# Optimization experiments

Measured on AMD Instinct MI355X. Metric: run time of the kernel, lower is better.

## Reference

```python
import jax, jax.numpy as jnp
import numpy as np

B, S, I, H, L, O = 32, 512, 1024, 1024, 3, 1024


def setup_inputs() -> dict:
    key = jax.random.key(0)
    ks = jax.random.split(key, 13)
    sc = 1.0 / np.sqrt(H)
    w = lambda k, shape: (jax.random.normal(k, shape, dtype=jnp.float32) * sc)
    return {
        "x": jax.random.normal(ks[0], (B, S, I), dtype=jnp.float32),
        "h0": jax.random.normal(ks[1], (B, L, H), dtype=jnp.float32),
        "Wzi": w(ks[2], (L, H, I)),
        "Wzh": w(ks[3], (L, H, H)),
        "bzh": w(ks[4], (L, H)),
        "Wri": w(ks[5], (L, H, I)),
        "Wrh": w(ks[6], (L, H, H)),
        "brh": w(ks[7], (L, H)),
        "Wgi": w(ks[8], (L, H, I)),
        "Wgh": w(ks[9], (L, H, H)),
        "bgh": w(ks[10], (L, H)),
        "Wout": w(ks[11], (O, H)),
        "bout": w(ks[12], (O,)),
    }


def reference(x, h0, Wzi, Wzh, bzh, Wri, Wrh, brh, Wgi, Wgh, bgh, Wout, bout):
    n_layers = Wzi.shape[0]
    # carry: hidden per layer, shape (L, B, H)
    h_init = jnp.transpose(h0, (1, 0, 2))
    x_t_major = jnp.transpose(x, (1, 0, 2))  # (S, B, I)

    def step(h, x_t):
        inp = x_t
        new_h = []
        for l in range(n_layers):
            hl = h[l]
            z = jax.nn.sigmoid(inp @ Wzi[l].T + hl @ Wzh[l].T + bzh[l])
            r = jax.nn.sigmoid(inp @ Wri[l].T + hl @ Wrh[l].T + brh[l])
            g = jnp.tanh(inp @ Wgi[l].T + r * (hl @ Wgh[l].T + bgh[l]))
            hn = z * hl + (1.0 - z) * g  # update gate keeps old state
            new_h.append(hn)
            inp = hn
        out_t = inp @ Wout.T + bout
        return jnp.stack(new_h), out_t

    h_final, outs = jax.lax.scan(step, h_init, x_t_major)
    layer_output = jnp.transpose(outs, (1, 0, 2))   # (B, S, O)
    hidden_state = jnp.transpose(h_final, (1, 0, 2))  # (B, L, H)
    return layer_output, hidden_state
```

## Files before the change

kernel.cpp:

```cpp
#include <hip/hip_runtime.h>
#include <hip/hip_bf16.h>


#define NB 32
#define NS 512
#define NI 1024
#define NH 1024
#define NL 3
#define NO 1024

#define WGN 256
#define BLK 512
#define SLOTS 12
#define RPB 2096
#define ZROW 72
#define COFF (73 * RPB)
#define CPITCH 33
#define LDSB (COFF + 48 * CPITCH * 4)

#define GENB   (WGN * 32)
#define CLAIMB (GENB + 16 * 32)
#define DONEB  (CLAIMB + 16 * 32)
#define GFL_N  9472

using short8 = __attribute__((ext_vector_type(8))) short;
using floatx4 = __attribute__((ext_vector_type(4))) float;

static __device__ __forceinline__ float bf2f(unsigned short u) {
    union { unsigned int i; float f; } v;
    v.i = ((unsigned int)u) << 16;
    return v.f;
}

static __device__ __forceinline__ unsigned short f2bf(float f) {
    __hip_bfloat16 h = __float2bfloat16(f);
    union { __hip_bfloat16 h; unsigned short u; } v;
    v.h = h;
    return v.u;
}

static __device__ __forceinline__ void load8h(const unsigned short* p, float w[8]) {
    uint4 q = *(const uint4*)p;
    unsigned int u[4] = {q.x, q.y, q.z, q.w};
#pragma unroll
    for (int i = 0; i < 4; ++i) {
        w[2*i]   = __uint_as_float(u[i] << 16);
        w[2*i+1] = __uint_as_float(u[i] & 0xffff0000u);
    }
}

static __device__ __forceinline__ void load8f(const float* p, float w[8]) {
    float4 a = *(const float4*)p;
    float4 b = *(const float4*)(p + 4);
    w[0]=a.x; w[1]=a.y; w[2]=a.z; w[3]=a.w;
    w[4]=b.x; w[5]=b.y; w[6]=b.z; w[7]=b.w;
}

static __device__ __forceinline__ int xcc_id() {
    unsigned v;
    asm volatile("s_getreg_b32 %0, hwreg(20, 0, 32)" : "=s"(v));
    return (int)(v & 7);
}

__global__ void detect_kernel(const unsigned int* __restrict__ xw, int* __restrict__ flag) {
    __shared__ int cnt[256];
    int c = 0;
    for (int i = threadIdx.x; i < 1024; i += 256) {
        unsigned int e = (xw[i] >> 7) & 0xFFu;
        if (e >= 0x78u && e <= 0x84u) c++;
    }
    cnt[threadIdx.x] = c;
    __syncthreads();
    if (threadIdx.x == 0) {
        int s = 0;
        for (int i = 0; i < 256; ++i) s += cnt[i];
        *flag = (s < 512) ? 1 : 0;
    }
}

__global__ void init_act(const void* __restrict__ h0,
                         unsigned int* __restrict__ act,
                         unsigned int* __restrict__ gflags,
                         const int* __restrict__ flagp) {
    const int f32m = *flagp;
    const int idx = blockIdx.x * 256 + threadIdx.x;
    if (idx < GFL_N) gflags[idx] = 0u;
    if (idx >= NL * NB * NH) return;
    const int l = idx >> 15;
    const int b = (idx >> 10) & 31;
    const int j = idx & 1023;
    const size_t src = (size_t)b * NL * NH + (size_t)l * NH + j;
    float v = f32m ? ((const float*)h0)[src] : bf2f(((const unsigned short*)h0)[src]);
    unsigned short hi = f2bf(v);
    unsigned short lo = f2bf(v - bf2f(hi));
    const size_t dst = ((size_t)(l * 2 + 1) * NB + b) * NH + j;
    act[dst] = ((unsigned int)hi << 16) | lo;
}

template<int F32M>
__global__ __launch_bounds__(BLK, 2) void gru_persist(
    const void* __restrict__ x,
    const void* __restrict__ Wzi_, const void* __restrict__ Wzh_, const void* __restrict__ bzh_,
    const void* __restrict__ Wri_, const void* __restrict__ Wrh_, const void* __restrict__ brh_,
    const void* __restrict__ Wgi_, const void* __restrict__ Wgh_, const void* __restrict__ bgh_,
    void* __restrict__ dout,
    unsigned int* __restrict__ act,
    float* __restrict__ stfin,
    const int* __restrict__ flagp,
    unsigned int* __restrict__ gflags)
{
    if (*flagp != F32M) return;

    extern __shared__ char lds[];
    float* clds = (float*)(lds + COFF);

    const int tid  = threadIdx.x;
    const int wg   = blockIdx.x;
    const int lane = tid & 63;
    const int wid  = tid >> 6;
    const int Mtile = wid & 1;
    const int khalf = wid >> 1;
    const int n16  = lane & 15;
    const int q4   = lane >> 4;

    const int slot0 = wg * SLOTS;

    {
        const void* Wmats[6] = {Wzi_, Wzh_, Wri_, Wrh_, Wgi_, Wgh_};
        if (F32M) {
            for (int idx = tid; idx < 72 * 256; idx += BLK) {
                const int r = idx >> 8, c4 = (idx & 255) * 4;
                const int slot = slot0 + r / 6, g = r % 6;
                const int layer = slot >> 10, j = slot & 1023;
                const float* src = (const float*)Wmats[g] + (size_t)layer * NH * NI + (size_t)j * NI + c4;
                float4 f = *(const float4*)src;
                unsigned short* dst = (unsigned short*)(lds + r * RPB + c4 * 2);
                dst[0] = f2bf(f.x); dst[1] = f2bf(f.y); dst[2] = f2bf(f.z); dst[3] = f2bf(f.w);
            }
        } else {
            for (int idx = tid; idx < 72 * 128; idx += BLK) {
                const int r = idx >> 7, c8 = (idx & 127) * 8;
                const int slot = slot0 + r / 6, g = r % 6;
                const int layer = slot >> 10, j = slot & 1023;
                const unsigned short* src = (const unsigned short*)Wmats[g] + (size_t)layer * NH * NI + (size_t)j * NI + c8;
                *(uint4*)(lds + r * RPB + c8 * 2) = *(const uint4*)src;
            }
        }
        unsigned int* z = (unsigned int*)(lds + ZROW * RPB);
        for (int c = tid; c < RPB / 4; c += BLK) z[c] = 0u;
        for (int i = tid; i < 48 * CPITCH; i += BLK) clds[i] = 0.f;
    }

    int eci = 0, eb = 0, elg = 0, ej = 0;
    float ebz = 0.f, ebr = 0.f, ebg = 0.f, ehp = 0.f;
    if (tid < NB * SLOTS) {
        eci = tid % SLOTS; eb = tid / SLOTS;
        const int slot = slot0 + eci;
        elg = slot >> 10; ej = slot & 1023;
        const size_t bidx = (size_t)elg * NH + ej;
        if (F32M) {
            ebz = ((const float*)bzh_)[bidx];
            ebr = ((const float*)brh_)[bidx];
            ebg = ((const float*)bgh_)[bidx];
        } else {
            ebz = bf2f(((const unsigned short*)bzh_)[bidx]);
            ebr = bf2f(((const unsigned short*)brh_)[bidx]);
            ebg = bf2f(((const unsigned short*)bgh_)[bidx]);
        }
    }

    const int lay0 = slot0 >> 10;
    const int lay1 = (slot0 + SLOTS - 1) >> 10;
    const int ngroups = (lay0 == lay1) ? 1 : 2;
    const int n0 = (ngroups == 1) ? SLOTS : (1024 - (slot0 & 1023));

    const int myxcd = xcc_id();
    const bool isl0 = (lay0 == 0);
    const int mb = Mtile * 16 + n16;

    short8 XH[8], XL[8];
    auto xprefetch = [&](int t) {
        if (F32M) {
            const float* xb = (const float*)x + ((size_t)mb * NS + t) * NI + khalf * 256 + q4 * 8;
#pragma unroll
            for (int ks = 0; ks < 8; ++ks) {
                float f[8];
                load8f(xb + ks * 32, f);
#pragma unroll
                for (int e = 0; e < 8; ++e) {
                    unsigned short h = f2bf(f[e]);
                    XH[ks][e] = (short)h;
                    XL[ks][e] = (short)f2bf(f[e] - bf2f(h));
                }
            }
        } else {
            const unsigned short* xb = (const unsigned short*)x + ((size_t)mb * NS + t) * NI + khalf * 256 + q4 * 8;
#pragma unroll
            for (int ks = 0; ks < 8; ++ks)
                XH[ks] = *(const short8*)(xb + ks * 32);
        }
    };
    if (isl0) xprefetch(0);

    __syncthreads();

    for (int s = 0; s < NS + NL - 1; ++s) {
        floatx4 acc[3];
#pragma unroll
        for (int nt = 0; nt < 3; ++nt) acc[nt] = (floatx4){0.f, 0.f, 0.f, 0.f};

        for (int grp = 0; grp < ngroups; ++grp) {
            const int lg = (grp == 0) ? lay0 : lay1;
            const int t = s - lg;
            if (t < 0 || t >= NS) continue;
            const int ntLo = (grp == 0) ? 0 : ((4 * n0) >> 4);
            const int ntHi = (grp == 0) ? (ngroups == 1 ? 2 : ((4 * n0) >> 4) - 1) : 2;

            for (int phase = 0; phase < 2; ++phase) {
                int brow[3];
#pragma unroll
                for (int nt = 0; nt < 3; ++nt) {
                    const int v = nt * 16 + n16;
                    const int ci = v >> 2, g = v & 3;
                    int r;
                    if (phase == 0) r = (g == 3) ? ZROW : ci * 6 + ((g == 2) ? 4 : g * 2);
                    else            r = (g == 2) ? ZROW : ci * 6 + ((g == 3) ? 5 : g * 2 + 1);
                    brow[nt] = r;
                }

                const bool isx = (phase == 0 && lg == 0);
                const bool dolo = isx ? (F32M != 0) : true;

                short8 AH[8], AL[8];
                if (isx) {
#pragma unroll
                    for (int ks = 0; ks < 8; ++ks) { AH[ks] = XH[ks]; if (F32M) AL[ks] = XL[ks]; }
                } else {
                    const int src_l = (phase == 0) ? lg - 1 : lg;
                    const int src_p = (phase == 0) ? (t & 1) : ((t - 1) & 1);
                    const size_t ab = ((size_t)(src_l * 2 + src_p) * NB + mb) * NH + khalf * 256 + q4 * 8;
                    const uint4* ap = (const uint4*)(act + ab);
                    uint4 qq[16];
#pragma unroll
                    for (int ks = 0; ks < 8; ++ks) {
                        qq[2*ks]   = ap[ks * 8];
                        qq[2*ks+1] = ap[ks * 8 + 1];
                    }
#pragma unroll
                    for (int ks = 0; ks < 8; ++ks) {
                        unsigned int c[8] = {qq[2*ks].x, qq[2*ks].y, qq[2*ks].z, qq[2*ks].w,
                                             qq[2*ks+1].x, qq[2*ks+1].y, qq[2*ks+1].z, qq[2*ks+1].w};
#pragma unroll
                        for (int e = 0; e < 8; ++e) {
                            AH[ks][e] = (short)(c[e] >> 16);
                            AL[ks][e] = (short)(c[e] & 0xffffu);
                        }
                    }
                }

#pragma unroll
                for (int ks = 0; ks < 8; ++ks) {
                    const int k0 = khalf * 256 + ks * 32;
#pragma unroll
                    for (int nt = 0; nt < 3; ++nt) {
                        if (nt < ntLo || nt > ntHi) continue;
                        const short8 bf = *(const short8*)(lds + brow[nt] * RPB + k0 * 2 + q4 * 16);
                        acc[nt] = __builtin_amdgcn_mfma_f32_16x16x32_bf16(AH[ks], bf, acc[nt], 0, 0, 0);
                        if (dolo)
                            acc[nt] = __builtin_amdgcn_mfma_f32_16x16x32_bf16(AL[ks], bf, acc[nt], 0, 0, 0);
                    }
                }
            }
        }

        {
            const int mbase = Mtile * 16 + q4 * 4;
#pragma unroll
            for (int nt = 0; nt < 3; ++nt) {
                const int vcol = nt * 16 + n16;
#pragma unroll
                for (int r = 0; r < 4; ++r)
                    atomicAdd(&clds[vcol * CPITCH + mbase + r], acc[nt][r]);
            }
        }
        __syncthreads();

        if (tid < NB * SLOTS) {
            const int t = s - elg;
            if (t >= 0 && t < NS) {
                const float zp = clds[(eci * 4 + 0) * CPITCH + eb];
                const float rp = clds[(eci * 4 + 1) * CPITCH + eb];
                const float gi = clds[(eci * 4 + 2) * CPITCH + eb];
                const float gh = clds[(eci * 4 + 3) * CPITCH + eb];
                clds[(eci * 4 + 0) * CPITCH + eb] = 0.f;
                clds[(eci * 4 + 1) * CPITCH + eb] = 0.f;
                clds[(eci * 4 + 2) * CPITCH + eb] = 0.f;
                clds[(eci * 4 + 3) * CPITCH + eb] = 0.f;
                float hp;
                if (t == 0) {
                    const size_t hoff = ((size_t)(elg * 2 + 1) * NB + eb) * NH + ej;
                    const unsigned int pv = act[hoff];
                    hp = bf2f((unsigned short)(pv >> 16)) + bf2f((unsigned short)(pv & 0xffffu));
                } else {
                    hp = ehp;
                }
                const float z = 1.f / (1.f + expf(-(zp + ebz)));
                const float r = 1.f / (1.f + expf(-(rp + ebr)));
                const float g = tanhf(gi + r * (gh + ebg));
                const float hn = z * hp + (1.f - z) * g;
                ehp = hn;
                const unsigned short hi = f2bf(hn);
                const unsigned short lo = f2bf(hn - bf2f(hi));
                const size_t woff = ((size_t)(elg * 2 + (t & 1)) * NB + eb) * NH + ej;
                __hip_atomic_store(&act[woff], ((unsigned int)hi << 16) | lo,
                                   __ATOMIC_RELAXED, __HIP_MEMORY_SCOPE_AGENT);
                if (elg == 2) {
                    const size_t o = ((size_t)eb * NS + t) * NO + ej;
                    if (F32M) ((float*)dout)[o] = hn;
                    else      ((unsigned short*)dout)[o] = f2bf(hn);
                }
                if (t == NS - 1)
                    stfin[((size_t)elg * NB + eb) * NH + ej] = hn;
            }
        }

        __syncthreads();
        if (tid == 0)
            __hip_atomic_store(&gflags[wg * 32], (unsigned int)(s + 1),
                               __ATOMIC_RELAXED, __HIP_MEMORY_SCOPE_AGENT);

        if (isl0 && (s + 1) < NS) xprefetch(s + 1);

        if (wg == 0) {
            if (tid < WGN) {
                while (__hip_atomic_load(&gflags[tid * 32], __ATOMIC_RELAXED,
                                         __HIP_MEMORY_SCOPE_AGENT) <= (unsigned int)s)
                    __builtin_amdgcn_s_sleep(1);
            }
            __syncthreads();
            if (tid < 16)
                __hip_atomic_store(&gflags[GENB + tid * 32], (unsigned int)(s + 1),
                                   __ATOMIC_RELAXED, __HIP_MEMORY_SCOPE_AGENT);
        } else {
            if (tid == 0) {
                while (__hip_atomic_load(&gflags[GENB + (wg >> 4) * 32], __ATOMIC_RELAXED,
                                         __HIP_MEMORY_SCOPE_AGENT) <= (unsigned int)s)
                    __builtin_amdgcn_s_sleep(1);
            }
        }
        if (tid == 0) {
            const unsigned tag = (unsigned)(s + 1);
            unsigned* claim = &gflags[CLAIMB + (myxcd * 2 + (s & 1)) * 32];
            unsigned old = __hip_atomic_exchange(claim, tag,
                                                 __ATOMIC_RELAXED, __HIP_MEMORY_SCOPE_AGENT);
            if (old != tag) {
                __builtin_amdgcn_fence(__ATOMIC_ACQUIRE, "agent");
                __hip_atomic_store(&gflags[DONEB + myxcd * 32], tag,
                                   __ATOMIC_RELAXED, __HIP_MEMORY_SCOPE_AGENT);
            } else {
                while (__hip_atomic_load(&gflags[DONEB + myxcd * 32], __ATOMIC_RELAXED,
                                         __HIP_MEMORY_SCOPE_AGENT) <= (unsigned int)s)
                    __builtin_amdgcn_s_sleep(1);
                asm volatile("buffer_inv" ::: "memory");
            }
            __builtin_amdgcn_sched_barrier(0);
        }
        __syncthreads();
    }
}

__global__ void init_kernel(const void* __restrict__ h0, float* __restrict__ st,
                            const int* __restrict__ flagp) {
    const int f32m = *flagp;
    const int idx = blockIdx.x * 256 + threadIdx.x;
    if (idx >= NL * NB * NH) return;
    const int l = idx >> 15;
    const int b = (idx >> 10) & 31;
    const int j = idx & 1023;
    const size_t src = (size_t)b * NL * NH + (size_t)l * NH + j;
    st[idx] = f32m ? ((const float*)h0)[src] : bf2f(((const unsigned short*)h0)[src]);
}

__global__ __launch_bounds__(256) void gru_layer(
    const void*  __restrict__ x,
    const float* __restrict__ inp,
    const float* __restrict__ hprev,
    float*       __restrict__ hnew,
    void*        __restrict__ h2out,
    const void* __restrict__ Wzi_, const void* __restrict__ Wzh_, const void* __restrict__ bzh_,
    const void* __restrict__ Wri_, const void* __restrict__ Wrh_, const void* __restrict__ brh_,
    const void* __restrict__ Wgi_, const void* __restrict__ Wgh_, const void* __restrict__ bgh_,
    const int* __restrict__ flagp, int tl, int isX)
{
    __shared__ float s_in[NB][129];
    __shared__ float s_h [NB][129];
    __shared__ float s_red[256][6];

    const int f32m = *flagp;
    const int t = tl & 0xFFFF;
    const int l = tl >> 16;
    const int tid = threadIdx.x;
    const int b   = tid & 31;
    const int jl  = (tid >> 5) & 1;
    const int ks  = tid >> 6;
    const int j   = blockIdx.x * 2 + jl;

    const size_t wIl = (size_t)l * NH * NI + (size_t)j * NI;
    const size_t bl  = (size_t)l * NH + j;

    float azi = 0.f, azh = 0.f, ari = 0.f, arh = 0.f, agi = 0.f, agh = 0.f;

    for (int kc = 0; kc < 8; ++kc) {
        const int k0 = kc * 128;
        __syncthreads();
        for (int idx = tid; idx < NB * 128; idx += 256) {
            const int r = idx >> 7, c = idx & 127;
            float vi;
            if (isX) {
                const size_t xo = (size_t)r * NS * NI + (size_t)t * NI + (k0 + c);
                vi = f32m ? ((const float*)x)[xo] : bf2f(((const unsigned short*)x)[xo]);
            } else {
                vi = inp[r * NH + k0 + c];
            }
            s_in[r][c] = vi;
            s_h [r][c] = hprev[r * NH + k0 + c];
        }
        __syncthreads();

        const int cbase = ks * 32;
#pragma unroll
        for (int q8 = 0; q8 < 4; ++q8) {
            const int c = cbase + q8 * 8;
            const int k = k0 + c;
            float wz[8], wr[8], wg[8], vz[8], vr[8], vg[8];
            if (f32m) {
                load8f((const float*)Wzi_ + wIl + k, wz);
                load8f((const float*)Wri_ + wIl + k, wr);
                load8f((const float*)Wgi_ + wIl + k, wg);
                load8f((const float*)Wzh_ + wIl + k, vz);
                load8f((const float*)Wrh_ + wIl + k, vr);
                load8f((const float*)Wgh_ + wIl + k, vg);
            } else {
                load8h((const unsigned short*)Wzi_ + wIl + k, wz);
                load8h((const unsigned short*)Wri_ + wIl + k, wr);
                load8h((const unsigned short*)Wgi_ + wIl + k, wg);
                load8h((const unsigned short*)Wzh_ + wIl + k, vz);
                load8h((const unsigned short*)Wrh_ + wIl + k, vr);
                load8h((const unsigned short*)Wgh_ + wIl + k, vg);
            }
            float ai[8], ah[8];
#pragma unroll
            for (int q = 0; q < 8; ++q) { ai[q] = s_in[b][c + q]; ah[q] = s_h[b][c + q]; }
#pragma unroll
            for (int q = 0; q < 8; ++q) {
                azi = fmaf(wz[q], ai[q], azi);
                ari = fmaf(wr[q], ai[q], ari);
                agi = fmaf(wg[q], ai[q], agi);
                azh = fmaf(vz[q], ah[q], azh);
                arh = fmaf(vr[q], ah[q], arh);
                agh = fmaf(vg[q], ah[q], agh);
            }
        }
    }

    s_red[tid][0] = azi; s_red[tid][1] = azh; s_red[tid][2] = ari;
    s_red[tid][3] = arh; s_red[tid][4] = agi; s_red[tid][5] = agh;
    __syncthreads();

    if (ks == 0) {
#pragma unroll
        for (int w = 1; w < 4; ++w) {
            azi += s_red[tid + 64*w][0]; azh += s_red[tid + 64*w][1];
            ari += s_red[tid + 64*w][2]; arh += s_red[tid + 64*w][3];
            agi += s_red[tid + 64*w][4]; agh += s_red[tid + 64*w][5];
        }
        const float bz = f32m ? ((const float*)bzh_)[bl] : bf2f(((const unsigned short*)bzh_)[bl]);
        const float br = f32m ? ((const float*)brh_)[bl] : bf2f(((const unsigned short*)brh_)[bl]);
        const float bg = f32m ? ((const float*)bgh_)[bl] : bf2f(((const unsigned short*)bgh_)[bl]);
        const float z = 1.f / (1.f + expf(-(azi + azh + bz)));
        const float r = 1.f / (1.f + expf(-(ari + arh + br)));
        const float g = tanhf(agi + r * (agh + bg));
        const float hp = hprev[b * NH + j];
        const float hn = z * hp + (1.f - z) * g;
        hnew[b * NH + j] = hn;
        if (h2out) {
            const size_t off = (size_t)b * NS * NO + (size_t)t * NO + j;
            if (f32m) ((float*)h2out)[off] = hn;
            else      ((unsigned short*)h2out)[off] = f2bf(hn);
        }
    }
}

__global__ __launch_bounds__(256) void out_gemm(
    void* __restrict__ out, const void* __restrict__ Wout, const void* __restrict__ bout,
    const int* __restrict__ flagp)
{
    __shared__ float s_a[8][1024];
    const int f32m = *flagp;
    const int tid = threadIdx.x;
    const size_t row0 = (size_t)blockIdx.x * 8;

    for (int idx = tid; idx < 8 * 1024; idx += 256) {
        const int r = idx >> 10, c = idx & 1023;
        const size_t off = (row0 + r) * NO + c;
        s_a[r][c] = f32m ? ((const float*)out)[off] : bf2f(((const unsigned short*)out)[off]);
    }
    __syncthreads();

    float acc[4][8];
#pragma unroll
    for (int m = 0; m < 4; ++m)
#pragma unroll
        for (int r = 0; r < 8; ++r) acc[m][r] = 0.f;

    for (int k8 = 0; k8 < 128; ++k8) {
        const int k = k8 * 8;
        float wf[4][8];
#pragma unroll
        for (int m = 0; m < 4; ++m) {
            const size_t wo = (size_t)(tid + 256*m) * NH + k;
            if (f32m) load8f((const float*)Wout + wo, wf[m]);
            else      load8h((const unsigned short*)Wout + wo, wf[m]);
        }
#pragma unroll
        for (int r = 0; r < 8; ++r) {
            float a[8];
#pragma unroll
            for (int q = 0; q < 8; ++q) a[q] = s_a[r][k + q];
#pragma unroll
            for (int m = 0; m < 4; ++m)
#pragma unroll
                for (int q = 0; q < 8; ++q)
                    acc[m][r] = fmaf(wf[m][q], a[q], acc[m][r]);
        }
    }

#pragma unroll
    for (int m = 0; m < 4; ++m) {
        const int jj = tid + 256*m;
        const float bj = f32m ? ((const float*)bout)[jj] : bf2f(((const unsigned short*)bout)[jj]);
#pragma unroll
        for (int r = 0; r < 8; ++r) {
            const size_t off = (row0 + r) * NO + jj;
            const float v = acc[m][r] + bj;
            if (f32m) ((float*)out)[off] = v;
            else      ((unsigned short*)out)[off] = f2bf(v);
        }
    }
}

__global__ void tail_kernel(const float* __restrict__ st, void* __restrict__ out,
                            const int* __restrict__ flagp)
{
    const int f32m = *flagp;
    const int idx = blockIdx.x * 256 + threadIdx.x;
    if (idx >= NL * NB * NH) return;
    const int l = idx >> 15;
    const int b = (idx >> 10) & 31;
    const int j = idx & 1023;
    const size_t dst = (size_t)NB * NS * NO + (size_t)b * NL * NH + (size_t)l * NH + j;
    if (f32m) ((float*)out)[dst] = st[idx];
    else      ((unsigned short*)out)[dst] = f2bf(st[idx]);
}

extern "C" void kernel_launch(void* const* d_in, const int* in_sizes, int n_in,
                              void* d_out, int out_size, void* d_ws, size_t ws_size,
                              hipStream_t stream)
{
    const void* x    = d_in[0];
    const void* h0   = d_in[1];
    const void* Wzi  = d_in[2];
    const void* Wzh  = d_in[3];
    const void* bzh  = d_in[4];
    const void* Wri  = d_in[5];
    const void* Wrh  = d_in[6];
    const void* brh  = d_in[7];
    const void* Wgi  = d_in[8];
    const void* Wgh  = d_in[9];
    const void* bgh  = d_in[10];
    const void* Wout = d_in[11];
    const void* bout = d_in[12];

    char* w = (char*)d_ws;
    float* st            = (float*)w;
    int*   flag          = (int*)(w + 786432);
    unsigned int* act    = (unsigned int*)(w + 786464);
    unsigned int* gflags = (unsigned int*)(w + 1572992);
    auto stp = [&](int p, int l) { return st + ((size_t)(p * NL + l)) * NB * NH; };

    detect_kernel<<<1, 256, 0, stream>>>((const unsigned int*)x, flag);
    init_act<<<(NL*NB*NH + 255)/256, 256, 0, stream>>>(h0, act, gflags, flag);

    (void)hipFuncSetAttribute((const void*)&gru_persist<1>,
                              hipFuncAttributeMaxDynamicSharedMemorySize, LDSB);
    (void)hipFuncSetAttribute((const void*)&gru_persist<0>,
                              hipFuncAttributeMaxDynamicSharedMemorySize, LDSB);
    (void)hipGetLastError();
    gru_persist<1><<<WGN, BLK, LDSB, stream>>>(
        x, Wzi, Wzh, bzh, Wri, Wrh, brh, Wgi, Wgh, bgh,
        d_out, act, st, flag, gflags);
    gru_persist<0><<<WGN, BLK, LDSB, stream>>>(
        x, Wzi, Wzh, bzh, Wri, Wrh, brh, Wgi, Wgh, bgh,
        d_out, act, st, flag, gflags);
    hipError_t perr = hipGetLastError();

    if (perr != hipSuccess) {
        init_kernel<<<(NL*NB*NH + 255)/256, 256, 0, stream>>>(h0, st, flag);
        for (int t = 0; t < NS; ++t) {
            const int pr = t & 1, pw = 1 - pr;
            for (int l = 0; l < NL; ++l) {
                gru_layer<<<512, 256, 0, stream>>>(
                    x,
                    l == 0 ? st : stp(pw, l - 1),
                    stp(pr, l),
                    stp(pw, l),
                    l == 2 ? d_out : (void*)nullptr,
                    Wzi, Wzh, bzh, Wri, Wrh, brh, Wgi, Wgh, bgh,
                    flag, t | (l << 16), l == 0 ? 1 : 0);
            }
        }
    }

    out_gemm<<<NB * NS / 8, 256, 0, stream>>>(d_out, Wout, bout, flag);
    tail_kernel<<<(NL*NB*NH + 255)/256, 256, 0, stream>>>(st, d_out, flag);
}
```

Measured before the change: 12.59 ms.

## Stage activations into per-XCD copies with cooperative copy and XCD barrier

After each step's grid barrier, the workgroups on each XCD cooperatively copy the freshly written activation slabs from the shared act buffer into a per-XCD staging buffer. An XCD-local counting barrier replaces the old claim/done scheme, and MFMA operand loads then read from the XCD-local copy, aiming to keep them in that XCD's L2 instead of fetching across dies. The cost is an extra copy pass plus one more barrier per step. It also adds a prologue step and ticket counters, and needs a larger workspace; if the workspace is too small it falls back to the per-layer path.

```diff
diff --git a/kernel.cpp b/kernel.cpp
--- a/kernel.cpp
+++ b/kernel.cpp
@@ -16,12 +16,15 @@
 #define ZROW 72
 #define COFF (73 * RPB)
 #define CPITCH 33
-#define LDSB (COFF + 48 * CPITCH * 4)
+#define SHTK (COFF + 48 * CPITCH * 4)
+#define LDSB (SHTK + 16)
 
 #define GENB   (WGN * 32)
-#define CLAIMB (GENB + 16 * 32)
-#define DONEB  (CLAIMB + 16 * 32)
-#define GFL_N  9472
+#define CNTB   (GENB + 16 * 32)
+#define XBARB  (CNTB + 8 * 32)
+#define GFL_N  (XBARB + 8 * 32)
+
+#define STAGE_U32 196608
 
 using short8 = __attribute__((ext_vector_type(8))) short;
 using floatx4 = __attribute__((ext_vector_type(4))) float;
@@ -105,6 +108,7 @@
     const void* __restrict__ Wgi_, const void* __restrict__ Wgh_, const void* __restrict__ bgh_,
     void* __restrict__ dout,
     unsigned int* __restrict__ act,
+    unsigned int* __restrict__ stage,
     float* __restrict__ stfin,
     const int* __restrict__ flagp,
     unsigned int* __restrict__ gflags)
@@ -113,6 +117,7 @@
 
     extern __shared__ char lds[];
     float* clds = (float*)(lds + COFF);
+    int* sh_tk = (int*)(lds + SHTK);
 
     const int tid  = threadIdx.x;
     const int wg   = blockIdx.x;
@@ -124,6 +129,12 @@
     const int q4   = lane >> 4;
 
     const int slot0 = wg * SLOTS;
+    const int myxcd = xcc_id();
+    unsigned int* const stageX = stage + (size_t)myxcd * STAGE_U32;
+
+    if (tid == 0)
+        sh_tk[0] = (int)__hip_atomic_fetch_add(&gflags[CNTB + myxcd * 32], 1u,
+                                               __ATOMIC_RELAXED, __HIP_MEMORY_SCOPE_AGENT);
 
     {
         const void* Wmats[6] = {Wzi_, Wzh_, Wri_, Wrh_, Wgi_, Wgh_};
@@ -174,7 +185,6 @@
     const int ngroups = (lay0 == lay1) ? 1 : 2;
     const int n0 = (ngroups == 1) ? SLOTS : (1024 - (slot0 & 1023));
 
-    const int myxcd = xcc_id();
     const bool isl0 = (lay0 == 0);
     const int mb = Mtile * 16 + n16;
 
@@ -200,133 +210,136 @@
                 XH[ks] = *(const short8*)(xb + ks * 32);
         }
     };
-    if (isl0) xprefetch(0);
 
     __syncthreads();
-
-    for (int s = 0; s < NS + NL - 1; ++s) {
-        floatx4 acc[3];
-#pragma unroll
-        for (int nt = 0; nt < 3; ++nt) acc[nt] = (floatx4){0.f, 0.f, 0.f, 0.f};
-
-        for (int grp = 0; grp < ngroups; ++grp) {
-            const int lg = (grp == 0) ? lay0 : lay1;
-            const int t = s - lg;
-            if (t < 0 || t >= NS) continue;
-            const int ntLo = (grp == 0) ? 0 : ((4 * n0) >> 4);
-            const int ntHi = (grp == 0) ? (ngroups == 1 ? 2 : ((4 * n0) >> 4) - 1) : 2;
-
-            for (int phase = 0; phase < 2; ++phase) {
-                int brow[3];
-#pragma unroll
-                for (int nt = 0; nt < 3; ++nt) {
-                    const int v = nt * 16 + n16;
-                    const int ci = v >> 2, g = v & 3;
-                    int r;
-                    if (phase == 0) r = (g == 3) ? ZROW : ci * 6 + ((g == 2) ? 4 : g * 2);
-                    else            r = (g == 2) ? ZROW : ci * 6 + ((g == 3) ? 5 : g * 2 + 1);
-                    brow[nt] = r;
-                }
-
-                const bool isx = (phase == 0 && lg == 0);
-                const bool dolo = isx ? (F32M != 0) : true;
-
-                short8 AH[8], AL[8];
-                if (isx) {
-#pragma unroll
-                    for (int ks = 0; ks < 8; ++ks) { AH[ks] = XH[ks]; if (F32M) AL[ks] = XL[ks]; }
-                } else {
-                    const int src_l = (phase == 0) ? lg - 1 : lg;
-                    const int src_p = (phase == 0) ? (t & 1) : ((t - 1) & 1);
-                    const size_t ab = ((size_t)(src_l * 2 + src_p) * NB + mb) * NH + khalf * 256 + q4 * 8;
-                    const uint4* ap = (const uint4*)(act + ab);
-                    uint4 qq[16];
+    const int myticket = sh_tk[0];
+    int myT = 1;
+
+    for (int s = -1; s < NS + NL - 1; ++s) {
+        if (s >= 0) {
+            floatx4 acc[3];
+#pragma unroll
+            for (int nt = 0; nt < 3; ++nt) acc[nt] = (floatx4){0.f, 0.f, 0.f, 0.f};
+
+            for (int grp = 0; grp < ngroups; ++grp) {
+                const int lg = (grp == 0) ? lay0 : lay1;
+                const int t = s - lg;
+                if (t < 0 || t >= NS) continue;
+                const int ntLo = (grp == 0) ? 0 : ((4 * n0) >> 4);
+                const int ntHi = (grp == 0) ? (ngroups == 1 ? 2 : ((4 * n0) >> 4) - 1) : 2;
+
+                for (int phase = 0; phase < 2; ++phase) {
+                    int brow[3];
+#pragma unroll
+                    for (int nt = 0; nt < 3; ++nt) {
+                        const int v = nt * 16 + n16;
+                        const int ci = v >> 2, g = v & 3;
+                        int r;
+                        if (phase == 0) r = (g == 3) ? ZROW : ci * 6 + ((g == 2) ? 4 : g * 2);
+                        else            r = (g == 2) ? ZROW : ci * 6 + ((g == 3) ? 5 : g * 2 + 1);
+                        brow[nt] = r;
+                    }
+
+                    const bool isx = (phase == 0 && lg == 0);
+                    const bool dolo = isx ? (F32M != 0) : true;
+
+                    short8 AH[8], AL[8];
+                    if (isx) {
+#pragma unroll
+                        for (int ks = 0; ks < 8; ++ks) { AH[ks] = XH[ks]; if (F32M) AL[ks] = XL[ks]; }
+                    } else {
+                        const int src_l = (phase == 0) ? lg - 1 : lg;
+                        const int src_p = (phase == 0) ? (t & 1) : ((t - 1) & 1);
+                        const size_t ab = ((size_t)(src_l * 2 + src_p) * NB + mb) * NH + khalf * 256 + q4 * 8;
+                        const uint4* ap = (const uint4*)(stageX + ab);
+                        uint4 qq[16];
+#pragma unroll
+                        for (int ks = 0; ks < 8; ++ks) {
+                            qq[2*ks]   = ap[ks * 8];
+                            qq[2*ks+1] = ap[ks * 8 + 1];
+                        }
+#pragma unroll
+                        for (int ks = 0; ks < 8; ++ks) {
+                            unsigned int c[8] = {qq[2*ks].x, qq[2*ks].y, qq[2*ks].z, qq[2*ks].w,
+                                                 qq[2*ks+1].x, qq[2*ks+1].y, qq[2*ks+1].z, qq[2*ks+1].w};
+#pragma unroll
+                            for (int e = 0; e < 8; ++e) {
+                                AH[ks][e] = (short)(c[e] >> 16);
+                                AL[ks][e] = (short)(c[e] & 0xffffu);
+                            }
+                        }
+                    }
+
 #pragma unroll
                     for (int ks = 0; ks < 8; ++ks) {
-                        qq[2*ks]   = ap[ks * 8];
-                        qq[2*ks+1] = ap[ks * 8 + 1];
-                    }
-#pragma unroll
-                    for (int ks = 0; ks < 8; ++ks) {
-                        unsigned int c[8] = {qq[2*ks].x, qq[2*ks].y, qq[2*ks].z, qq[2*ks].w,
-                                             qq[2*ks+1].x, qq[2*ks+1].y, qq[2*ks+1].z, qq[2*ks+1].w};
-#pragma unroll
-                        for (int e = 0; e < 8; ++e) {
-                            AH[ks][e] = (short)(c[e] >> 16);
-                            AL[ks][e] = (short)(c[e] & 0xffffu);
+                        const int k0 = khalf * 256 + ks * 32;
+#pragma unroll
+                        for (int nt = 0; nt < 3; ++nt) {
+                            if (nt < ntLo || nt > ntHi) continue;
+                            const short8 bf = *(const short8*)(lds + brow[nt] * RPB + k0 * 2 + q4 * 16);
+                            acc[nt] = __builtin_amdgcn_mfma_f32_16x16x32_bf16(AH[ks], bf, acc[nt], 0, 0, 0);
+                            if (dolo)
+                                acc[nt] = __builtin_amdgcn_mfma_f32_16x16x32_bf16(AL[ks], bf, acc[nt], 0, 0, 0);
                         }
                     }
                 }
-
-#pragma unroll
-                for (int ks = 0; ks < 8; ++ks) {
-                    const int k0 = khalf * 256 + ks * 32;
-#pragma unroll
-                    for (int nt = 0; nt < 3; ++nt) {
-                        if (nt < ntLo || nt > ntHi) continue;
-                        const short8 bf = *(const short8*)(lds + brow[nt] * RPB + k0 * 2 + q4 * 16);
-                        acc[nt] = __builtin_amdgcn_mfma_f32_16x16x32_bf16(AH[ks], bf, acc[nt], 0, 0, 0);
-                        if (dolo)
-                            acc[nt] = __builtin_amdgcn_mfma_f32_16x16x32_bf16(AL[ks], bf, acc[nt], 0, 0, 0);
+            }
+
+            {
+                const int mbase = Mtile * 16 + q4 * 4;
+#pragma unroll
+                for (int nt = 0; nt < 3; ++nt) {
+                    const int vcol = nt * 16 + n16;
+#pragma unroll
+                    for (int r = 0; r < 4; ++r)
+                        atomicAdd(&clds[vcol * CPITCH + mbase + r], acc[nt][r]);
+                }
+            }
+            __syncthreads();
+
+            if (tid < NB * SLOTS) {
+                const int t = s - elg;
+                if (t >= 0 && t < NS) {
+                    const float zp = clds[(eci * 4 + 0) * CPITCH + eb];
+                    const float rp = clds[(eci * 4 + 1) * CPITCH + eb];
+                    const float gi = clds[(eci * 4 + 2) * CPITCH + eb];
+                    const float gh = clds[(eci * 4 + 3) * CPITCH + eb];
+                    clds[(eci * 4 + 0) * CPITCH + eb] = 0.f;
+                    clds[(eci * 4 + 1) * CPITCH + eb] = 0.f;
+                    clds[(eci * 4 + 2) * CPITCH + eb] = 0.f;
+                    clds[(eci * 4 + 3) * CPITCH + eb] = 0.f;
+                    float hp;
+                    if (t == 0) {
+                        const size_t hoff = ((size_t)(elg * 2 + 1) * NB + eb) * NH + ej;
+                        const unsigned int pv = stageX[hoff];
+                        hp = bf2f((unsigned short)(pv >> 16)) + bf2f((unsigned short)(pv & 0xffffu));
+                    } else {
+                        hp = ehp;
                     }
+                    const float z = 1.f / (1.f + expf(-(zp + ebz)));
+                    const float r = 1.f / (1.f + expf(-(rp + ebr)));
+                    const float g = tanhf(gi + r * (gh + ebg));
+                    const float hn = z * hp + (1.f - z) * g;
+                    ehp = hn;
+                    const unsigned short hi = f2bf(hn);
+                    const unsigned short lo = f2bf(hn - bf2f(hi));
+                    const size_t woff = ((size_t)(elg * 2 + (t & 1)) * NB + eb) * NH + ej;
+                    __hip_atomic_store(&act[woff], ((unsigned int)hi << 16) | lo,
+                                       __ATOMIC_RELAXED, __HIP_MEMORY_SCOPE_AGENT);
+                    if (elg == 2) {
+                        const size_t o = ((size_t)eb * NS + t) * NO + ej;
+                        if (F32M) ((float*)dout)[o] = hn;
+                        else      ((unsigned short*)dout)[o] = f2bf(hn);
+                    }
+                    if (t == NS - 1)
+                        stfin[((size_t)elg * NB + eb) * NH + ej] = hn;
                 }
-            }
-        }
-
-        {
-            const int mbase = Mtile * 16 + q4 * 4;
-#pragma unroll
-            for (int nt = 0; nt < 3; ++nt) {
-                const int vcol = nt * 16 + n16;
-#pragma unroll
-                for (int r = 0; r < 4; ++r)
-                    atomicAdd(&clds[vcol * CPITCH + mbase + r], acc[nt][r]);
-            }
-        }
-        __syncthreads();
-
-        if (tid < NB * SLOTS) {
-            const int t = s - elg;
-            if (t >= 0 && t < NS) {
-                const float zp = clds[(eci * 4 + 0) * CPITCH + eb];
-                const float rp = clds[(eci * 4 + 1) * CPITCH + eb];
-                const float gi = clds[(eci * 4 + 2) * CPITCH + eb];
-                const float gh = clds[(eci * 4 + 3) * CPITCH + eb];
-                clds[(eci * 4 + 0) * CPITCH + eb] = 0.f;
-                clds[(eci * 4 + 1) * CPITCH + eb] = 0.f;
-                clds[(eci * 4 + 2) * CPITCH + eb] = 0.f;
-                clds[(eci * 4 + 3) * CPITCH + eb] = 0.f;
-                float hp;
-                if (t == 0) {
-                    const size_t hoff = ((size_t)(elg * 2 + 1) * NB + eb) * NH + ej;
-                    const unsigned int pv = act[hoff];
-                    hp = bf2f((unsigned short)(pv >> 16)) + bf2f((unsigned short)(pv & 0xffffu));
-                } else {
-                    hp = ehp;
-                }
-                const float z = 1.f / (1.f + expf(-(zp + ebz)));
-                const float r = 1.f / (1.f + expf(-(rp + ebr)));
-                const float g = tanhf(gi + r * (gh + ebg));
-                const float hn = z * hp + (1.f - z) * g;
-                ehp = hn;
-                const unsigned short hi = f2bf(hn);
-                const unsigned short lo = f2bf(hn - bf2f(hi));
-                const size_t woff = ((size_t)(elg * 2 + (t & 1)) * NB + eb) * NH + ej;
-                __hip_atomic_store(&act[woff], ((unsigned int)hi << 16) | lo,
-                                   __ATOMIC_RELAXED, __HIP_MEMORY_SCOPE_AGENT);
-                if (elg == 2) {
-                    const size_t o = ((size_t)eb * NS + t) * NO + ej;
-                    if (F32M) ((float*)dout)[o] = hn;
-                    else      ((unsigned short*)dout)[o] = f2bf(hn);
-                }
-                if (t == NS - 1)
-                    stfin[((size_t)elg * NB + eb) * NH + ej] = hn;
             }
         }
 
         __syncthreads();
         if (tid == 0)
-            __hip_atomic_store(&gflags[wg * 32], (unsigned int)(s + 1),
+            __hip_atomic_store(&gflags[wg * 32], (unsigned int)(s + 2),
                                __ATOMIC_RELAXED, __HIP_MEMORY_SCOPE_AGENT);
 
         if (isl0 && (s + 1) < NS) xprefetch(s + 1);
@@ -334,35 +347,63 @@
         if (wg == 0) {
             if (tid < WGN) {
                 while (__hip_atomic_load(&gflags[tid * 32], __ATOMIC_RELAXED,
-                                         __HIP_MEMORY_SCOPE_AGENT) <= (unsigned int)s)
+                                         __HIP_MEMORY_SCOPE_AGENT) <= (unsigned int)(s + 1))
                     __builtin_amdgcn_s_sleep(1);
             }
             __syncthreads();
             if (tid < 16)
-                __hip_atomic_store(&gflags[GENB + tid * 32], (unsigned int)(s + 1),
+                __hip_atomic_store(&gflags[GENB + tid * 32], (unsigned int)(s + 2),
                                    __ATOMIC_RELAXED, __HIP_MEMORY_SCOPE_AGENT);
         } else {
             if (tid == 0) {
                 while (__hip_atomic_load(&gflags[GENB + (wg >> 4) * 32], __ATOMIC_RELAXED,
-                                         __HIP_MEMORY_SCOPE_AGENT) <= (unsigned int)s)
+                                         __HIP_MEMORY_SCOPE_AGENT) <= (unsigned int)(s + 1))
                     __builtin_amdgcn_s_sleep(1);
             }
         }
+        __syncthreads();
+
+        if (s == -1) {
+            if (tid == 0)
+                sh_tk[1] = (int)__hip_atomic_load(&gflags[CNTB + myxcd * 32],
+                                                  __ATOMIC_RELAXED, __HIP_MEMORY_SCOPE_AGENT);
+            __syncthreads();
+            myT = sh_tk[1];
+        }
+
+        {
+            int slabs[6]; int nslab = 0;
+            if (s < 0) {
+                slabs[0]=0; slabs[1]=1; slabs[2]=2; slabs[3]=3; slabs[4]=4; slabs[5]=5;
+                nslab = 6;
+            } else {
+#pragma unroll
+                for (int l = 0; l < NL; ++l) {
+                    const int tl = s - l;
+                    if (tl >= 0 && tl < NS) slabs[nslab++] = l * 2 + (tl & 1);
+                }
+            }
+            const int nv = nslab << 13;
+            for (int i = myticket * BLK + tid; i < nv; i += myT * BLK) {
+                const int k = i >> 13;
+                const size_t so = ((size_t)slabs[k] << 15) + (size_t)(i & 8191) * 4;
+                const unsigned long long* sp = (const unsigned long long*)(act + so);
+                const unsigned long long a = __hip_atomic_load(sp,     __ATOMIC_RELAXED, __HIP_MEMORY_SCOPE_AGENT);
+                const unsigned long long b = __hip_atomic_load(sp + 1, __ATOMIC_RELAXED, __HIP_MEMORY_SCOPE_AGENT);
+                *(unsigned long long*)(stageX + so)     = a;
+                *(unsigned long long*)(stageX + so + 2) = b;
+            }
+        }
+        __syncthreads();
+
         if (tid == 0) {
-            const unsigned tag = (unsigned)(s + 1);
-            unsigned* claim = &gflags[CLAIMB + (myxcd * 2 + (s & 1)) * 32];
-            unsigned old = __hip_atomic_exchange(claim, tag,
-                                                 __ATOMIC_RELAXED, __HIP_MEMORY_SCOPE_AGENT);
-            if (old != tag) {
-                __builtin_amdgcn_fence(__ATOMIC_ACQUIRE, "agent");
-                __hip_atomic_store(&gflags[DONEB + myxcd * 32], tag,
+            __hip_atomic_fetch_add(&gflags[XBARB + myxcd * 32], 1u,
                                    __ATOMIC_RELAXED, __HIP_MEMORY_SCOPE_AGENT);
-            } else {
-                while (__hip_atomic_load(&gflags[DONEB + myxcd * 32], __ATOMIC_RELAXED,
-                                         __HIP_MEMORY_SCOPE_AGENT) <= (unsigned int)s)
-                    __builtin_amdgcn_s_sleep(1);
-                asm volatile("buffer_inv" ::: "memory");
-            }
+            const unsigned target = (unsigned)myT * (unsigned)(s + 2);
+            while (__hip_atomic_load(&gflags[XBARB + myxcd * 32], __ATOMIC_RELAXED,
+                                     __HIP_MEMORY_SCOPE_AGENT) < target)
+                __builtin_amdgcn_s_sleep(1);
+            asm volatile("buffer_inv\n\ts_waitcnt vmcnt(0)" ::: "memory");
             __builtin_amdgcn_sched_barrier(0);
         }
         __syncthreads();
@@ -586,25 +627,30 @@
     int*   flag          = (int*)(w + 786432);
     unsigned int* act    = (unsigned int*)(w + 786464);
     unsigned int* gflags = (unsigned int*)(w + 1572992);
+    unsigned int* stage  = (unsigned int*)(w + 2097152);
     auto stp = [&](int p, int l) { return st + ((size_t)(p * NL + l)) * NB * NH; };
 
     detect_kernel<<<1, 256, 0, stream>>>((const unsigned int*)x, flag);
     init_act<<<(NL*NB*NH + 255)/256, 256, 0, stream>>>(h0, act, gflags, flag);
 
-    (void)hipFuncSetAttribute((const void*)&gru_persist<1>,
-                              hipFuncAttributeMaxDynamicSharedMemorySize, LDSB);
-    (void)hipFuncSetAttribute((const void*)&gru_persist<0>,
-                              hipFuncAttributeMaxDynamicSharedMemorySize, LDSB);
-    (void)hipGetLastError();
-    gru_persist<1><<<WGN, BLK, LDSB, stream>>>(
-        x, Wzi, Wzh, bzh, Wri, Wrh, brh, Wgi, Wgh, bgh,
-        d_out, act, st, flag, gflags);
-    gru_persist<0><<<WGN, BLK, LDSB, stream>>>(
-        x, Wzi, Wzh, bzh, Wri, Wrh, brh, Wgi, Wgh, bgh,
-        d_out, act, st, flag, gflags);
-    hipError_t perr = hipGetLastError();
-
-    if (perr != hipSuccess) {
+    const bool ws_ok = (ws_size == 0)  || (ws_size >= 8912896);
+    hipError_t perr = hipSuccess;
+    if (ws_ok) {
+        (void)hipFuncSetAttribute((const void*)&gru_persist<1>,
+                                  hipFuncAttributeMaxDynamicSharedMemorySize, LDSB);
+        (void)hipFuncSetAttribute((const void*)&gru_persist<0>,
+                                  hipFuncAttributeMaxDynamicSharedMemorySize, LDSB);
+        (void)hipGetLastError();
+        gru_persist<1><<<WGN, BLK, LDSB, stream>>>(
+            x, Wzi, Wzh, bzh, Wri, Wrh, brh, Wgi, Wgh, bgh,
+            d_out, act, stage, st, flag, gflags);
+        gru_persist<0><<<WGN, BLK, LDSB, stream>>>(
+            x, Wzi, Wzh, bzh, Wri, Wrh, brh, Wgi, Wgh, bgh,
+            d_out, act, stage, st, flag, gflags);
+        perr = hipGetLastError();
+    }
+
+    if (!ws_ok || perr != hipSuccess) {
         init_kernel<<<(NL*NB*NH + 255)/256, 256, 0, stream>>>(h0, st, flag);
         for (int t = 0; t < NS; ++t) {
             const int pr = t & 1, pw = 1 - pr;
```

Result: slower. 13.56 ms (+7.7%).
